# Performance work log

Measured on AMD Instinct MI355X. Metric: run time of the kernel, lower is better.

The kernel has to match this reference:

```python
import jax, jax.numpy as jnp
import numpy as np

HIDDEN = 4096
NUM_EXPERTS = 64
TOKENS = 16384
TOP_K = 2


def setup_inputs() -> dict:
    key = jax.random.key(0)
    kx, kw = jax.random.split(key)
    x = jax.random.normal(kx, (TOKENS, HIDDEN), dtype=jnp.float32)
    # router gate weight, as in nn.Parameter(torch.randn(num_experts, hidden_size))
    weight = jax.random.normal(kw, (NUM_EXPERTS, HIDDEN), dtype=jnp.float32)
    return {"x": x, "weight": weight}


def reference(x, weight):
    # logits = F.linear(x, weight)  -> [tokens, num_experts]
    logits = jnp.einsum("th,eh->te", x, weight)
    # top-2 experts per token, then softmax over the 2 selected logits
    top_vals, selected_experts = jax.lax.top_k(logits, TOP_K)  # [tokens, 2]
    weights = jax.nn.softmax(top_vals, axis=-1)
    return weights, selected_experts
```

## Files before the change

### kernel.cpp

```cpp
#include <hip/hip_runtime.h>
#include <math.h>

#define TOKENS 16384
#define HIDDEN 4096
#define NEXP   64
#define NSL    8
#define KSL    (HIDDEN / NSL)
#define TOKB   128
#define NCH    (KSL / 32)

typedef _Float16 half8 __attribute__((ext_vector_type(8)));
typedef float    f32x4 __attribute__((ext_vector_type(4)));

__global__ void w_prep(const float* __restrict__ W,
                       _Float16* __restrict__ Wh, _Float16* __restrict__ Wl) {
    int idx = blockIdx.x * blockDim.x + threadIdx.x;
    int e = idx >> 12;
    int k = idx & 4095;
    float v = W[idx];
    _Float16 h = (_Float16)v;
    _Float16 l = (_Float16)(v - (float)h);
    size_t dst = (((size_t)(k >> 5) * NEXP) + e) * 32 + (k & 31);
    Wh[dst] = h;
    Wl[dst] = l;
}

__device__ __forceinline__ void split8(const float4& p0, const float4& p1,
                                       half8& h, half8& l) {
    const float v[8] = {p0.x, p0.y, p0.z, p0.w, p1.x, p1.y, p1.z, p1.w};
    #pragma unroll
    for (int j = 0; j < 8; ++j) {
        _Float16 hi = (_Float16)v[j];
        h[j] = hi;
        l[j] = (_Float16)(v[j] - (float)hi);
    }
}

__global__ __launch_bounds__(256, 4) void router_mfma(
    const float* __restrict__ x, const _Float16* __restrict__ Wh,
    const _Float16* __restrict__ Wl, float* __restrict__ partial)
{
    const int tid  = threadIdx.x;
    const int lane = tid & 63;
    const int wv   = tid >> 6;
    const int e16  = lane & 15;
    const int quad = lane >> 4;

    const int tok0 = blockIdx.x * TOKB + wv * 32;
    const int sl   = blockIdx.y;
    const int kb0  = sl * NCH;

    f32x4 accA[4], accB[4];
    #pragma unroll
    for (int n = 0; n < 4; ++n) {
        accA[n] = (f32x4){0.f, 0.f, 0.f, 0.f};
        accB[n] = (f32x4){0.f, 0.f, 0.f, 0.f};
    }

    const float* xpA = x + (size_t)(tok0 + e16) * HIDDEN + sl * KSL + quad * 8;
    const float* xpB = xpA + (size_t)16 * HIDDEN;

    float4 pA0 = *(const float4*)(xpA),     pA1 = *(const float4*)(xpA + 4);
    float4 pB0 = *(const float4*)(xpB),     pB1 = *(const float4*)(xpB + 4);

    for (int c = 0; c < NCH; ++c) {
        const size_t bo = (((size_t)(kb0 + c) * NEXP) + e16) * 32 + quad * 8;
        half8 bh[4], bl[4];
        #pragma unroll
        for (int n = 0; n < 4; ++n) {
            bh[n] = *reinterpret_cast<const half8*>(Wh + bo + (size_t)n * 16 * 32);
            bl[n] = *reinterpret_cast<const half8*>(Wl + bo + (size_t)n * 16 * 32);
        }

        half8 ahA, alA, ahB, alB;
        split8(pA0, pA1, ahA, alA);
        split8(pB0, pB1, ahB, alB);
        if (c + 1 < NCH) {
            pA0 = *(const float4*)(xpA + (c + 1) * 32);
            pA1 = *(const float4*)(xpA + (c + 1) * 32 + 4);
            pB0 = *(const float4*)(xpB + (c + 1) * 32);
            pB1 = *(const float4*)(xpB + (c + 1) * 32 + 4);
        }

        #pragma unroll
        for (int n = 0; n < 4; ++n)
            accA[n] = __builtin_amdgcn_mfma_f32_16x16x32_f16(alA, bh[n], accA[n], 0, 0, 0);
        #pragma unroll
        for (int n = 0; n < 4; ++n)
            accB[n] = __builtin_amdgcn_mfma_f32_16x16x32_f16(alB, bh[n], accB[n], 0, 0, 0);
        #pragma unroll
        for (int n = 0; n < 4; ++n)
            accA[n] = __builtin_amdgcn_mfma_f32_16x16x32_f16(ahA, bl[n], accA[n], 0, 0, 0);
        #pragma unroll
        for (int n = 0; n < 4; ++n)
            accB[n] = __builtin_amdgcn_mfma_f32_16x16x32_f16(ahB, bl[n], accB[n], 0, 0, 0);
        #pragma unroll
        for (int n = 0; n < 4; ++n)
            accA[n] = __builtin_amdgcn_mfma_f32_16x16x32_f16(ahA, bh[n], accA[n], 0, 0, 0);
        #pragma unroll
        for (int n = 0; n < 4; ++n)
            accB[n] = __builtin_amdgcn_mfma_f32_16x16x32_f16(ahB, bh[n], accB[n], 0, 0, 0);
    }

    #pragma unroll
    for (int n = 0; n < 4; ++n) {
        float* pb = partial + ((size_t)sl * NEXP + n * 16 + e16) * TOKENS
                  + tok0 + quad * 4;
        *reinterpret_cast<float4*>(pb) =
            make_float4(accA[n][0], accA[n][1], accA[n][2], accA[n][3]);
        *reinterpret_cast<float4*>(pb + 16) =
            make_float4(accB[n][0], accB[n][1], accB[n][2], accB[n][3]);
    }
}

__global__ void reduce_topk(const float* __restrict__ partial,
                            float* __restrict__ out)
{
    int t = blockIdx.x * blockDim.x + threadIdx.x;
    float v1 = -INFINITY, v2 = -INFINITY;
    int i1 = 0, i2 = 0;
    #pragma unroll 4
    for (int e = 0; e < NEXP; ++e) {
        float v = 0.f;
        #pragma unroll
        for (int s = 0; s < NSL; ++s)
            v += partial[((size_t)s * NEXP + e) * TOKENS + t];
        if (v > v1)      { v2 = v1; i2 = i1; v1 = v; i1 = e; }
        else if (v > v2) { v2 = v;  i2 = e; }
    }
    float e2 = expf(v2 - v1);
    float d  = 1.f / (1.f + e2);
    out[t * 2 + 0] = d;
    out[t * 2 + 1] = e2 * d;
    out[2 * TOKENS + t * 2 + 0] = (float)i1;
    out[2 * TOKENS + t * 2 + 1] = (float)i2;
}

extern "C" void kernel_launch(void* const* d_in, const int* in_sizes, int n_in,
                              void* d_out, int out_size, void* d_ws, size_t ws_size,
                              hipStream_t stream) {
    const float* x = (const float*)d_in[0];
    const float* W = (const float*)d_in[1];
    float* out = (float*)d_out;

    _Float16* Wh = (_Float16*)d_ws;
    _Float16* Wl = Wh + (size_t)NEXP * HIDDEN;
    float* partial = (float*)((char*)d_ws + 2 * (size_t)NEXP * HIDDEN * sizeof(_Float16));

    w_prep<<<(NEXP * HIDDEN) / 256, 256, 0, stream>>>(W, Wh, Wl);
    dim3 grid(TOKENS / TOKB, NSL);
    router_mfma<<<grid, 256, 0, stream>>>(x, Wh, Wl, partial);
    reduce_topk<<<TOKENS / 128, 128, 0, stream>>>(partial, out);
}
```

Before: 404.7 us.

## Fuse split-K reduction and top-2 softmax into router GEMM via LDS

Each block now owns 32 tokens and splits the hidden dimension across its 4 waves instead of across grid slices. The partial logits are reduced in shared memory and top-2 softmax runs in the same kernel, so the global partial buffer and the separate reduce launch go away. This removes the round trip of 8 partial slices through global memory, but each wave now loops over 1024 K elements serially. Occupancy also changes, with 512 blocks of 256 threads, launch bounds lowered to 2, and about 36KB of LDS per block.

Result: faster. 392.6 us (-3.0%).

```diff
diff --git a/kernel.cpp b/kernel.cpp
--- a/kernel.cpp
+++ b/kernel.cpp
@@ -4,9 +4,9 @@
 #define TOKENS 16384
 #define HIDDEN 4096
 #define NEXP   64
-#define NSL    8
-#define KSL    (HIDDEN / NSL)
-#define TOKB   128
+#define TOKB   32
+#define WAVES  4
+#define KSL    (HIDDEN / WAVES)
 #define NCH    (KSL / 32)
 
 typedef _Float16 half8 __attribute__((ext_vector_type(8)));
@@ -36,19 +36,20 @@
     }
 }
 
-__global__ __launch_bounds__(256, 4) void router_mfma(
+__global__ __launch_bounds__(256, 2) void router_fused(
     const float* __restrict__ x, const _Float16* __restrict__ Wh,
-    const _Float16* __restrict__ Wl, float* __restrict__ partial)
+    const _Float16* __restrict__ Wl, float* __restrict__ out)
 {
+    __shared__ float lds[WAVES][NEXP][36];
+
     const int tid  = threadIdx.x;
     const int lane = tid & 63;
     const int wv   = tid >> 6;
     const int e16  = lane & 15;
     const int quad = lane >> 4;
 
-    const int tok0 = blockIdx.x * TOKB + wv * 32;
-    const int sl   = blockIdx.y;
-    const int kb0  = sl * NCH;
+    const int tok0 = blockIdx.x * TOKB;
+    const int kb0  = wv * NCH;
 
     f32x4 accA[4], accB[4];
     #pragma unroll
@@ -57,7 +58,7 @@
         accB[n] = (f32x4){0.f, 0.f, 0.f, 0.f};
     }
 
-    const float* xpA = x + (size_t)(tok0 + e16) * HIDDEN + sl * KSL + quad * 8;
+    const float* xpA = x + (size_t)(tok0 + e16) * HIDDEN + wv * KSL + quad * 8;
     const float* xpB = xpA + (size_t)16 * HIDDEN;
 
     float4 pA0 = *(const float4*)(xpA),     pA1 = *(const float4*)(xpA + 4);
@@ -104,36 +105,43 @@
 
     #pragma unroll
     for (int n = 0; n < 4; ++n) {
-        float* pb = partial + ((size_t)sl * NEXP + n * 16 + e16) * TOKENS
-                  + tok0 + quad * 4;
-        *reinterpret_cast<float4*>(pb) =
-            make_float4(accA[n][0], accA[n][1], accA[n][2], accA[n][3]);
-        *reinterpret_cast<float4*>(pb + 16) =
-            make_float4(accB[n][0], accB[n][1], accB[n][2], accB[n][3]);
+        *(f32x4*)&lds[wv][n * 16 + e16][quad * 4]      = accA[n];
+        *(f32x4*)&lds[wv][n * 16 + e16][16 + quad * 4] = accB[n];
     }
-}
+    __syncthreads();
 
-__global__ void reduce_topk(const float* __restrict__ partial,
-                            float* __restrict__ out)
-{
-    int t = blockIdx.x * blockDim.x + threadIdx.x;
-    float v1 = -INFINITY, v2 = -INFINITY;
-    int i1 = 0, i2 = 0;
-    #pragma unroll 4
-    for (int e = 0; e < NEXP; ++e) {
-        float v = 0.f;
+    {
+        const int e = tid >> 2;
+        const int q = tid & 3;
+        f32x4 s0 = (f32x4){0.f, 0.f, 0.f, 0.f};
+        f32x4 s1 = (f32x4){0.f, 0.f, 0.f, 0.f};
         #pragma unroll
-        for (int s = 0; s < NSL; ++s)
-            v += partial[((size_t)s * NEXP + e) * TOKENS + t];
-        if (v > v1)      { v2 = v1; i2 = i1; v1 = v; i1 = e; }
-        else if (v > v2) { v2 = v;  i2 = e; }
+        for (int w = 0; w < WAVES; ++w) {
+            s0 += *(const f32x4*)&lds[w][e][q * 8];
+            s1 += *(const f32x4*)&lds[w][e][q * 8 + 4];
+        }
+        *(f32x4*)&lds[0][e][q * 8]     = s0;
+        *(f32x4*)&lds[0][e][q * 8 + 4] = s1;
     }
-    float e2 = expf(v2 - v1);
-    float d  = 1.f / (1.f + e2);
-    out[t * 2 + 0] = d;
-    out[t * 2 + 1] = e2 * d;
-    out[2 * TOKENS + t * 2 + 0] = (float)i1;
-    out[2 * TOKENS + t * 2 + 1] = (float)i2;
+    __syncthreads();
+
+    if (tid < TOKB) {
+        float v1 = -INFINITY, v2 = -INFINITY;
+        int i1 = 0, i2 = 0;
+        #pragma unroll 8
+        for (int e = 0; e < NEXP; ++e) {
+            float v = lds[0][e][tid];
+            if (v > v1)      { v2 = v1; i2 = i1; v1 = v; i1 = e; }
+            else if (v > v2) { v2 = v;  i2 = e; }
+        }
+        float e2 = expf(v2 - v1);
+        float d  = 1.f / (1.f + e2);
+        int t = tok0 + tid;
+        out[t * 2 + 0] = d;
+        out[t * 2 + 1] = e2 * d;
+        out[2 * TOKENS + t * 2 + 0] = (float)i1;
+        out[2 * TOKENS + t * 2 + 1] = (float)i2;
+    }
 }
 
 extern "C" void kernel_launch(void* const* d_in, const int* in_sizes, int n_in,
@@ -145,10 +153,7 @@
 
     _Float16* Wh = (_Float16*)d_ws;
     _Float16* Wl = Wh + (size_t)NEXP * HIDDEN;
-    float* partial = (float*)((char*)d_ws + 2 * (size_t)NEXP * HIDDEN * sizeof(_Float16));
 
     w_prep<<<(NEXP * HIDDEN) / 256, 256, 0, stream>>>(W, Wh, Wl);
-    dim3 grid(TOKENS / TOKB, NSL);
-    router_mfma<<<grid, 256, 0, stream>>>(x, Wh, Wl, partial);
-    reduce_topk<<<TOKENS / 128, 128, 0, stream>>>(partial, out);
+    router_fused<<<TOKENS / TOKB, 256, 0, stream>>>(x, Wh, Wl, out);
 }
```
